# Kernel tuning notes

Measured on AMD Instinct MI355X. Metric: run time of the kernel, lower is better.

## Reference

```python
import jax, jax.numpy as jnp
import numpy as np

N = 10000      # nodes
E = 320000     # edges (avg degree 32)
D = 512        # input features
H = 2048       # dim_hidden hard-coded in module
C = 40         # num_classes


def setup_inputs() -> dict:
    key = jax.random.key(0)
    k = jax.random.split(key, 4)
    x = jax.random.normal(k[0], (N, D), dtype=jnp.float32)
    edge_index = jax.random.randint(k[1], (2, E), 0, N)
    W1 = jax.random.normal(k[2], (D, H), dtype=jnp.float32) * (1.0 / np.sqrt(D))
    b1 = jnp.zeros((H,), jnp.float32)
    W2 = jax.random.normal(k[3], (H, C), dtype=jnp.float32) * (1.0 / np.sqrt(H))
    b2 = jnp.zeros((C,), jnp.float32)
    return {"x": x, "edge_index": edge_index, "W1": W1, "b1": b1, "W2": W2, "b2": b2}


def _sym_norm(edge_index, n):
    # GCN symmetric normalization with self-loops: deg includes the self loop.
    src, dst = edge_index[0], edge_index[1]
    deg = jnp.zeros((n,), jnp.float32).at[dst].add(1.0) + 1.0
    dinv = jax.lax.rsqrt(deg)
    return src, dst, dinv


def _propagate(h, src, dst, dinv):
    # out[i] = sum_{j->i} dinv[j]*dinv[i]*h[j]  +  dinv[i]^2 * h[i] (self loop)
    coef = (dinv[src] * dinv[dst])[:, None]            # [E,1]
    agg = jax.ops.segment_sum(h[src] * coef, dst, num_segments=h.shape[0])
    return agg + h * (dinv * dinv)[:, None]


def _gcn_conv(x, W, b, src, dst, dinv):
    # A_hat (X W) == (A_hat X) W; aggregate in the smaller feature dim.
    if W.shape[0] <= W.shape[1]:
        return _propagate(x, src, dst, dinv) @ W + b
    return _propagate(x @ W, src, dst, dinv) + b


def reference(x, edge_index, W1, b1, W2, b2):
    src, dst, dinv = _sym_norm(edge_index, x.shape[0])
    h = jax.nn.relu(_gcn_conv(x, W1, b1, src, dst, dinv))
    return _gcn_conv(h, W2, b2, src, dst, dinv)
```

## Files before the change

kernel.cpp:

```cpp
#include <hip/hip_runtime.h>
#include <stdint.h>

#define N_NODES 10000
#define N_EDGES 320000
#define D_IN    512
#define D_HID   2048
#define N_CLS   40
#define MP1     10112
#define HSTR    136

typedef float f32x4  __attribute__((ext_vector_type(4)));
typedef short bf16x8 __attribute__((ext_vector_type(8)));
typedef unsigned short us8 __attribute__((ext_vector_type(8)));

__device__ inline unsigned short f2bf(float f){
  unsigned int u = __float_as_uint(f);
  u += 0x7fffu + ((u >> 16) & 1u);
  return (unsigned short)(u >> 16);
}

__device__ inline float bf2f(unsigned short h){
  return __uint_as_float(((unsigned int)h) << 16);
}

__device__ inline void gl_lds16(const void* g, void* l){
  __builtin_amdgcn_global_load_lds((const __attribute__((address_space(1))) void*)g,
                                   (__attribute__((address_space(3))) void*)l, 16, 0, 0);
}

__global__ void k_prep0(const float* __restrict__ x, unsigned short* __restrict__ Xb,
                        const int* __restrict__ ei, int* __restrict__ deg){
  if (blockIdx.x < 2500){
    int idx = blockIdx.x*256 + threadIdx.x;
    const f32x4* x4 = (const f32x4*)x;
    f32x4 a = x4[idx*2], b = x4[idx*2+1];
    us8 o;
    o[0]=f2bf(a.x); o[1]=f2bf(a.y); o[2]=f2bf(a.z); o[3]=f2bf(a.w);
    o[4]=f2bf(b.x); o[5]=f2bf(b.y); o[6]=f2bf(b.z); o[7]=f2bf(b.w);
    *(us8*)(Xb + (size_t)idx*8) = o;
  } else {
    int e = (blockIdx.x - 2500)*256 + threadIdx.x;
    if (e < N_EDGES) atomicAdd(&deg[ei[N_EDGES + e]], 1);
  }
}

__global__ void k_scan(const int* __restrict__ deg, int* __restrict__ offsets,
                       int* __restrict__ cursor, float* __restrict__ dinv){
  __shared__ int sums[1024];
  const int t = threadIdx.x;
  const int CH = 10;
  int base = t*CH;
  int local[CH]; int s = 0;
  for (int j = 0; j < CH; j++){
    int v = (base + j < N_NODES) ? deg[base + j] : 0;
    local[j] = s; s += v;
    if (base + j < N_NODES) dinv[base + j] = rsqrtf((float)v + 1.0f);
  }
  sums[t] = s;
  __syncthreads();
  for (int off = 1; off < 1024; off <<= 1){
    int v = (t >= off) ? sums[t - off] : 0;
    __syncthreads();
    sums[t] += v;
    __syncthreads();
  }
  int pre = (t > 0) ? sums[t-1] : 0;
  for (int j = 0; j < CH; j++){
    int idx = base + j;
    if (idx < N_NODES){ int o = pre + local[j]; offsets[idx] = o; cursor[idx] = o; }
  }
}

__global__ void k_fill(const int* __restrict__ ei, int* __restrict__ cursor, int* __restrict__ csr_src){
  int e = blockIdx.x*256 + threadIdx.x;
  if (e < N_EDGES){
    int s = ei[e], d = ei[N_EDGES + e];
    int pos = atomicAdd(&cursor[d], 1);
    csr_src[pos] = s;
  }
}

__global__ __launch_bounds__(256) void k_gjoint(const unsigned short* __restrict__ Xb,
                          const int* __restrict__ csr_src,
                          const int* __restrict__ offsets, const int* __restrict__ deg,
                          const float* __restrict__ dinv, unsigned short* __restrict__ Pb,
                          const float* __restrict__ W1, unsigned short* __restrict__ Wt1,
                          const float* __restrict__ W2, unsigned short* __restrict__ Wt2){
  __shared__ float tile[32][33];
  if (blockIdx.x < 2500){
    const int w    = threadIdx.x >> 6;
    const int lane = threadIdx.x & 63;
    const int i    = blockIdx.x*4 + w;
    const float di = dinv[i];
    float acc[8];
    us8 xi = *(const us8*)(Xb + (size_t)i*D_IN + lane*8);
    const float dii = di*di;
    #pragma unroll
    for (int r = 0; r < 8; r++) acc[r] = dii * bf2f(xi[r]);
    const int start = offsets[i], cnt = deg[i];
    const unsigned short* Xl = Xb + lane*8;
    for (int c0 = 0; c0 < cnt; c0 += 64){
      int m = cnt - c0; if (m > 64) m = 64;
      int s = 0; float cf = 0.0f;
      if (lane < m){ s = csr_src[start + c0 + lane]; cf = dinv[s]*di; }
      int j = 0;
      for (; j + 8 <= m; j += 8){
        int   s0 = __shfl(s, j),   s1 = __shfl(s, j+1), s2 = __shfl(s, j+2), s3 = __shfl(s, j+3);
        int   s4 = __shfl(s, j+4), s5 = __shfl(s, j+5), s6 = __shfl(s, j+6), s7 = __shfl(s, j+7);
        float c0f = __shfl(cf, j),   c1f = __shfl(cf, j+1), c2f = __shfl(cf, j+2), c3f = __shfl(cf, j+3);
        float c4f = __shfl(cf, j+4), c5f = __shfl(cf, j+5), c6f = __shfl(cf, j+6), c7f = __shfl(cf, j+7);
        us8 x0 = *(const us8*)(Xl + (size_t)s0*D_IN);
        us8 x1 = *(const us8*)(Xl + (size_t)s1*D_IN);
        us8 x2 = *(const us8*)(Xl + (size_t)s2*D_IN);
        us8 x3 = *(const us8*)(Xl + (size_t)s3*D_IN);
        us8 x4 = *(const us8*)(Xl + (size_t)s4*D_IN);
        us8 x5 = *(const us8*)(Xl + (size_t)s5*D_IN);
        us8 x6 = *(const us8*)(Xl + (size_t)s6*D_IN);
        us8 x7 = *(const us8*)(Xl + (size_t)s7*D_IN);
        #pragma unroll
        for (int r = 0; r < 8; r++) acc[r] += c0f * bf2f(x0[r]);
        #pragma unroll
        for (int r = 0; r < 8; r++) acc[r] += c1f * bf2f(x1[r]);
        #pragma unroll
        for (int r = 0; r < 8; r++) acc[r] += c2f * bf2f(x2[r]);
        #pragma unroll
        for (int r = 0; r < 8; r++) acc[r] += c3f * bf2f(x3[r]);
        #pragma unroll
        for (int r = 0; r < 8; r++) acc[r] += c4f * bf2f(x4[r]);
        #pragma unroll
        for (int r = 0; r < 8; r++) acc[r] += c5f * bf2f(x5[r]);
        #pragma unroll
        for (int r = 0; r < 8; r++) acc[r] += c6f * bf2f(x6[r]);
        #pragma unroll
        for (int r = 0; r < 8; r++) acc[r] += c7f * bf2f(x7[r]);
      }
      for (; j < m; j++){
        int   sj = __shfl(s, j);
        float cj = __shfl(cf, j);
        us8 xr = *(const us8*)(Xl + (size_t)sj*D_IN);
        #pragma unroll
        for (int r = 0; r < 8; r++) acc[r] += cj * bf2f(xr[r]);
      }
    }
    us8 o;
    #pragma unroll
    for (int r = 0; r < 8; r++) o[r] = f2bf(acc[r]);
    *(us8*)(Pb + (size_t)i*D_IN + lane*8) = o;
  } else if (blockIdx.x < 2500 + 1024){
    const int bb = blockIdx.x - 2500;
    const int n0 = (bb & 63)*32, k0 = (bb >> 6)*32;
    const int tx = threadIdx.x & 31, ty = threadIdx.x >> 5;
    for (int i = 0; i < 32; i += 8)
      tile[ty+i][tx] = W1[(size_t)(k0+ty+i)*D_HID + n0+tx];
    __syncthreads();
    for (int i = 0; i < 32; i += 8)
      Wt1[(size_t)(n0+ty+i)*D_IN + k0+tx] = f2bf(tile[tx][ty+i]);
  } else {
    int idx = (blockIdx.x - 3524)*256 + threadIdx.x;
    if (idx < 48*D_HID){
      int n = idx >> 11, k = idx & (D_HID-1);
      Wt2[idx] = (n < N_CLS) ? f2bf(W2[k*N_CLS + n]) : (unsigned short)0;
    }
  }
}

__global__ __launch_bounds__(256, 4) void k_gemm1f(const unsigned short* __restrict__ Pb,
                                                   const unsigned short* __restrict__ Wt1,
                                                   const float* __restrict__ b1,
                                                   const unsigned short* __restrict__ Wt2,
                                                   float* __restrict__ Gp){
  __shared__ short smem[128*HSTR];
  short* Hs = smem;
  const int t    = threadIdx.x;
  const int lane = t & 63;
  const int wid  = t >> 6;
  const int wm   = (wid >> 1)*64, wn = (wid & 1)*64;
  const int m0   = blockIdx.y*128, n0 = blockIdx.x*128;
  const int arow = t >> 2;
  const int akof = ((t & 3) ^ ((t >> 3) & 3))*8;
  const int fr   = lane & 15;
  const int q    = lane >> 4;
  const int sq8  = (q ^ ((fr >> 1) & 3))*8;

  const unsigned short* ApA = Pb  + (size_t)(m0 +      arow)*D_IN + akof;
  const unsigned short* ApB = Pb  + (size_t)(m0 + 64 + arow)*D_IN + akof;
  const unsigned short* BpA = Wt1 + (size_t)(n0 +      arow)*D_IN + akof;
  const unsigned short* BpB = Wt1 + (size_t)(n0 + 64 + arow)*D_IN + akof;

  f32x4 acc[4][4] = {};
  {
    short* As = smem;       short* Bs = smem + 4096;
    gl_lds16(ApA, As + t*8);  gl_lds16(ApB, As + 2048 + t*8);
    gl_lds16(BpA, Bs + t*8);  gl_lds16(BpB, Bs + 2048 + t*8);
  }
  #pragma unroll
  for (int ks = 0; ks < 16; ks++){
    if (ks < 15){
      short* As = smem + ((ks+1)&1)*8192;
      short* Bs = As + 4096;
      const int kb = (ks+1)*32;
      gl_lds16(ApA + kb, As + t*8);  gl_lds16(ApB + kb, As + 2048 + t*8);
      gl_lds16(BpA + kb, Bs + t*8);  gl_lds16(BpB + kb, Bs + 2048 + t*8);
      asm volatile("" ::: "memory");
      __builtin_amdgcn_s_waitcnt(0x0F74);
    } else {
      asm volatile("" ::: "memory");
      __builtin_amdgcn_s_waitcnt(0x0F70);
    }
    __builtin_amdgcn_s_barrier();
    asm volatile("" ::: "memory");
    const short* As = smem + (ks&1)*8192;
    const short* Bs = As + 4096;
    bf16x8 a[4], b[4];
    #pragma unroll
    for (int i = 0; i < 4; i++) a[i] = *(const bf16x8*)(As + (wm + i*16 + fr)*32 + sq8);
    #pragma unroll
    for (int j = 0; j < 4; j++) b[j] = *(const bf16x8*)(Bs + (wn + j*16 + fr)*32 + sq8);
    #pragma unroll
    for (int i = 0; i < 4; i++)
      #pragma unroll
      for (int j = 0; j < 4; j++)
        acc[i][j] = __builtin_amdgcn_mfma_f32_16x16x32_bf16(a[i], b[j], acc[i][j], 0, 0, 0);
    asm volatile("" ::: "memory");
    __builtin_amdgcn_s_barrier();
    asm volatile("" ::: "memory");
  }
  #pragma unroll
  for (int j = 0; j < 4; j++){
    int col = wn + j*16 + fr;
    float bias = b1[n0 + col];
    #pragma unroll
    for (int i = 0; i < 4; i++){
      int rbase = wm + i*16 + q*4;
      f32x4 v = acc[i][j];
      #pragma unroll
      for (int r = 0; r < 4; r++){
        float h = fmaxf(v[r] + bias, 0.0f);
        Hs[(rbase + r)*HSTR + col] = (short)f2bf(h);
      }
    }
  }
  __syncthreads();
  f32x4 acc2[2][3] = {};
  for (int ks = 0; ks < 4; ks++){
    bf16x8 a2[2];
    #pragma unroll
    for (int i2 = 0; i2 < 2; i2++)
      a2[i2] = *(const bf16x8*)(Hs + (wid*32 + i2*16 + fr)*HSTR + ks*32 + q*8);
    #pragma unroll
    for (int j2 = 0; j2 < 3; j2++){
      bf16x8 b2 = *(const bf16x8*)(Wt2 + (size_t)(j2*16 + fr)*D_HID + n0 + ks*32 + q*8);
      #pragma unroll
      for (int i2 = 0; i2 < 2; i2++)
        acc2[i2][j2] = __builtin_amdgcn_mfma_f32_16x16x32_bf16(a2[i2], b2, acc2[i2][j2], 0, 0, 0);
    }
  }
  float* Gpp = Gp + (size_t)blockIdx.x*N_NODES*N_CLS;
  #pragma unroll
  for (int j2 = 0; j2 < 3; j2++){
    int col = j2*16 + fr;
    if (col < N_CLS){
      #pragma unroll
      for (int i2 = 0; i2 < 2; i2++){
        int rbase = m0 + wid*32 + i2*16 + q*4;
        f32x4 v = acc2[i2][j2];
        #pragma unroll
        for (int r = 0; r < 4; r++){
          int row = rbase + r;
          if (row < N_NODES)
            Gpp[(size_t)row*N_CLS + col] = v[r];
        }
      }
    }
  }
}

__global__ void k_reduceG(const float* __restrict__ Gp, float* __restrict__ G){
  int idx = blockIdx.x*256 + threadIdx.x;
  if (idx < N_NODES*N_CLS){
    float s = 0.0f;
    #pragma unroll
    for (int p = 0; p < 16; p++)
      s += Gp[(size_t)p*N_NODES*N_CLS + idx];
    G[idx] = s;
  }
}

__global__ void k_gather2(const float* __restrict__ G, const int* __restrict__ csr_src,
                          const int* __restrict__ offsets, const int* __restrict__ deg,
                          const float* __restrict__ dinv, const float* __restrict__ b2,
                          float* __restrict__ out){
  __shared__ int   ssrc[64];
  __shared__ float scoef[64];
  const int i = blockIdx.x;
  const int t = threadIdx.x;
  const float di = dinv[i];
  const int start = offsets[i], cnt = deg[i];
  float acc = 0.0f;
  if (t < N_CLS) acc = di*di * G[i*N_CLS + t];
  for (int c0 = 0; c0 < cnt; c0 += 64){
    int m = cnt - c0; if (m > 64) m = 64;
    if (t < m){
      int s = csr_src[start + c0 + t];
      ssrc[t] = s; scoef[t] = dinv[s]*di;
    }
    __syncthreads();
    if (t < N_CLS)
      for (int j = 0; j < m; j++)
        acc += scoef[j] * G[ssrc[j]*N_CLS + t];
    __syncthreads();
  }
  if (t < N_CLS) out[i*N_CLS + t] = acc + b2[t];
}

extern "C" void kernel_launch(void* const* d_in, const int* in_sizes, int n_in,
                              void* d_out, int out_size, void* d_ws, size_t ws_size,
                              hipStream_t stream){
  const float* x  = (const float*)d_in[0];
  const int*   ei = (const int*)d_in[1];
  const float* W1 = (const float*)d_in[2];
  const float* b1 = (const float*)d_in[3];
  const float* W2 = (const float*)d_in[4];
  const float* b2 = (const float*)d_in[5];
  float* out = (float*)d_out;

  char* ws = (char*)d_ws;
  size_t off = 0;
  auto alloc = [&](size_t bytes) -> void* {
    void* p = ws + off; off += (bytes + 255) & ~(size_t)255; return p;
  };
  int*   deg     = (int*)alloc((size_t)N_NODES*4);
  float* dinv    = (float*)alloc((size_t)N_NODES*4);
  int*   offsets = (int*)alloc((size_t)N_NODES*4);
  int*   cursor  = (int*)alloc((size_t)N_NODES*4);
  int*   csr     = (int*)alloc((size_t)N_EDGES*4);
  unsigned short* Xb  = (unsigned short*)alloc((size_t)N_NODES*D_IN*2);
  unsigned short* Pb  = (unsigned short*)alloc((size_t)MP1*D_IN*2);
  unsigned short* Wt1 = (unsigned short*)alloc((size_t)D_HID*D_IN*2);
  unsigned short* Wt2 = (unsigned short*)alloc((size_t)48*D_HID*2);
  float* G  = (float*)alloc((size_t)N_NODES*N_CLS*4);
  float* Gp = (float*)alloc((size_t)16*N_NODES*N_CLS*4);

  hipMemsetAsync(deg, 0, (size_t)N_NODES*4, stream);

  k_prep0<<<2500 + 1250, 256, 0, stream>>>(x, Xb, ei, deg);
  k_scan<<<1, 1024, 0, stream>>>(deg, offsets, cursor, dinv);
  k_fill<<<(N_EDGES+255)/256, 256, 0, stream>>>(ei, cursor, csr);
  k_gjoint<<<2500 + 1024 + 384, 256, 0, stream>>>(Xb, csr, offsets, deg, dinv, Pb,
                                                  W1, Wt1, W2, Wt2);
  k_gemm1f<<<dim3(D_HID/128, MP1/128), 256, 0, stream>>>(Pb, Wt1, b1, Wt2, Gp);
  k_reduceG<<<(N_NODES*N_CLS + 255)/256, 256, 0, stream>>>(Gp, G);
  k_gather2<<<N_NODES, 64, 0, stream>>>(G, csr, offsets, deg, dinv, b2, out);
}
```

Before: 217.4 us.

## Enlarge GEMM1 tile to 256x128 with 512 threads and drop offsets array

The first GEMM block tile grows from 128x128 with 4 waves to 256x128 with 8 waves. Each block now loads one shared 128-row B tile plus two A halves per k-step, so every Wt1 tile is reused across more rows and the number of global-to-LDS loads per output element falls. The padded row count grows from 10112 to 10240 to fit the larger tile, and the epilogue's shared-memory H staging buffer doubles in size. Separately, the scan kernel no longer writes an offsets array: the gather kernels rebuild each node's start as the post-fill cursor minus its degree, which saves one store and one buffer.

Result: no change. 215.3 us (-0.9%).

```diff
diff --git a/kernel.cpp b/kernel.cpp
--- a/kernel.cpp
+++ b/kernel.cpp
@@ -6,7 +6,7 @@
 #define D_IN    512
 #define D_HID   2048
 #define N_CLS   40
-#define MP1     10112
+#define MP2     10240
 #define HSTR    136
 
 typedef float f32x4  __attribute__((ext_vector_type(4)));
@@ -44,17 +44,23 @@
   }
 }
 
-__global__ void k_scan(const int* __restrict__ deg, int* __restrict__ offsets,
-                       int* __restrict__ cursor, float* __restrict__ dinv){
+__global__ void k_scan(const int* __restrict__ deg, int* __restrict__ cursor,
+                       float* __restrict__ dinv){
+  __shared__ int sdeg[N_NODES];
   __shared__ int sums[1024];
   const int t = threadIdx.x;
+  for (int j = t; j < N_NODES; j += 1024){
+    int v = deg[j];
+    sdeg[j] = v;
+    dinv[j] = rsqrtf((float)v + 1.0f);
+  }
+  __syncthreads();
   const int CH = 10;
   int base = t*CH;
   int local[CH]; int s = 0;
   for (int j = 0; j < CH; j++){
-    int v = (base + j < N_NODES) ? deg[base + j] : 0;
+    int v = (base + j < N_NODES) ? sdeg[base + j] : 0;
     local[j] = s; s += v;
-    if (base + j < N_NODES) dinv[base + j] = rsqrtf((float)v + 1.0f);
   }
   sums[t] = s;
   __syncthreads();
@@ -67,8 +73,10 @@
   int pre = (t > 0) ? sums[t-1] : 0;
   for (int j = 0; j < CH; j++){
     int idx = base + j;
-    if (idx < N_NODES){ int o = pre + local[j]; offsets[idx] = o; cursor[idx] = o; }
-  }
+    if (idx < N_NODES) sdeg[idx] = pre + local[j];
+  }
+  __syncthreads();
+  for (int j = t; j < N_NODES; j += 1024) cursor[j] = sdeg[j];
 }
 
 __global__ void k_fill(const int* __restrict__ ei, int* __restrict__ cursor, int* __restrict__ csr_src){
@@ -82,7 +90,7 @@
 
 __global__ __launch_bounds__(256) void k_gjoint(const unsigned short* __restrict__ Xb,
                           const int* __restrict__ csr_src,
-                          const int* __restrict__ offsets, const int* __restrict__ deg,
+                          const int* __restrict__ cursor, const int* __restrict__ deg,
                           const float* __restrict__ dinv, unsigned short* __restrict__ Pb,
                           const float* __restrict__ W1, unsigned short* __restrict__ Wt1,
                           const float* __restrict__ W2, unsigned short* __restrict__ Wt2){
@@ -97,7 +105,8 @@
     const float dii = di*di;
     #pragma unroll
     for (int r = 0; r < 8; r++) acc[r] = dii * bf2f(xi[r]);
-    const int start = offsets[i], cnt = deg[i];
+    const int cnt = deg[i];
+    const int start = cursor[i] - cnt;
     const unsigned short* Xl = Xb + lane*8;
     for (int c0 = 0; c0 < cnt; c0 += 64){
       int m = cnt - c0; if (m > 64) m = 64;
@@ -164,53 +173,53 @@
   }
 }
 
-__global__ __launch_bounds__(256, 4) void k_gemm1f(const unsigned short* __restrict__ Pb,
+__global__ __launch_bounds__(512, 4) void k_gemm1f(const unsigned short* __restrict__ Pb,
                                                    const unsigned short* __restrict__ Wt1,
                                                    const float* __restrict__ b1,
                                                    const unsigned short* __restrict__ Wt2,
                                                    float* __restrict__ Gp){
-  __shared__ short smem[128*HSTR];
+  __shared__ short smem[256*HSTR];
   short* Hs = smem;
   const int t    = threadIdx.x;
   const int lane = t & 63;
   const int wid  = t >> 6;
-  const int wm   = (wid >> 1)*64, wn = (wid & 1)*64;
-  const int m0   = blockIdx.y*128, n0 = blockIdx.x*128;
+  const int wm   = (wid >> 1)*64;
+  const int wn   = (wid & 1)*64;
+  const int m0   = blockIdx.y*256, n0 = blockIdx.x*128;
   const int arow = t >> 2;
   const int akof = ((t & 3) ^ ((t >> 3) & 3))*8;
   const int fr   = lane & 15;
   const int q    = lane >> 4;
   const int sq8  = (q ^ ((fr >> 1) & 3))*8;
 
-  const unsigned short* ApA = Pb  + (size_t)(m0 +      arow)*D_IN + akof;
-  const unsigned short* ApB = Pb  + (size_t)(m0 + 64 + arow)*D_IN + akof;
-  const unsigned short* BpA = Wt1 + (size_t)(n0 +      arow)*D_IN + akof;
-  const unsigned short* BpB = Wt1 + (size_t)(n0 + 64 + arow)*D_IN + akof;
+  const unsigned short* ApA = Pb  + (size_t)(m0 +       arow)*D_IN + akof;
+  const unsigned short* ApB = Pb  + (size_t)(m0 + 128 + arow)*D_IN + akof;
+  const unsigned short* BpA = Wt1 + (size_t)(n0 +       arow)*D_IN + akof;
 
   f32x4 acc[4][4] = {};
   {
-    short* As = smem;       short* Bs = smem + 4096;
-    gl_lds16(ApA, As + t*8);  gl_lds16(ApB, As + 2048 + t*8);
-    gl_lds16(BpA, Bs + t*8);  gl_lds16(BpB, Bs + 2048 + t*8);
+    gl_lds16(ApA, smem + t*8);
+    gl_lds16(ApB, smem + 4096 + t*8);
+    gl_lds16(BpA, smem + 8192 + t*8);
   }
   #pragma unroll
   for (int ks = 0; ks < 16; ks++){
     if (ks < 15){
-      short* As = smem + ((ks+1)&1)*8192;
-      short* Bs = As + 4096;
+      short* buf = smem + ((ks+1)&1)*12288;
       const int kb = (ks+1)*32;
-      gl_lds16(ApA + kb, As + t*8);  gl_lds16(ApB + kb, As + 2048 + t*8);
-      gl_lds16(BpA + kb, Bs + t*8);  gl_lds16(BpB + kb, Bs + 2048 + t*8);
+      gl_lds16(ApA + kb, buf + t*8);
+      gl_lds16(ApB + kb, buf + 4096 + t*8);
+      gl_lds16(BpA + kb, buf + 8192 + t*8);
       asm volatile("" ::: "memory");
-      __builtin_amdgcn_s_waitcnt(0x0F74);
+      __builtin_amdgcn_s_waitcnt(0x0F73);
     } else {
       asm volatile("" ::: "memory");
       __builtin_amdgcn_s_waitcnt(0x0F70);
     }
     __builtin_amdgcn_s_barrier();
     asm volatile("" ::: "memory");
-    const short* As = smem + (ks&1)*8192;
-    const short* Bs = As + 4096;
+    const short* As = smem + (ks&1)*12288;
+    const short* Bs = As + 8192;
     bf16x8 a[4], b[4];
     #pragma unroll
     for (int i = 0; i < 4; i++) a[i] = *(const bf16x8*)(As + (wm + i*16 + fr)*32 + sq8);
@@ -287,7 +296,7 @@
 }
 
 __global__ void k_gather2(const float* __restrict__ G, const int* __restrict__ csr_src,
-                          const int* __restrict__ offsets, const int* __restrict__ deg,
+                          const int* __restrict__ cursor, const int* __restrict__ deg,
                           const float* __restrict__ dinv, const float* __restrict__ b2,
                           float* __restrict__ out){
   __shared__ int   ssrc[64];
@@ -295,7 +304,8 @@
   const int i = blockIdx.x;
   const int t = threadIdx.x;
   const float di = dinv[i];
-  const int start = offsets[i], cnt = deg[i];
+  const int cnt = deg[i];
+  const int start = cursor[i] - cnt;
   float acc = 0.0f;
   if (t < N_CLS) acc = di*di * G[i*N_CLS + t];
   for (int c0 = 0; c0 < cnt; c0 += 64){
@@ -331,11 +341,10 @@
   };
   int*   deg     = (int*)alloc((size_t)N_NODES*4);
   float* dinv    = (float*)alloc((size_t)N_NODES*4);
-  int*   offsets = (int*)alloc((size_t)N_NODES*4);
   int*   cursor  = (int*)alloc((size_t)N_NODES*4);
   int*   csr     = (int*)alloc((size_t)N_EDGES*4);
   unsigned short* Xb  = (unsigned short*)alloc((size_t)N_NODES*D_IN*2);
-  unsigned short* Pb  = (unsigned short*)alloc((size_t)MP1*D_IN*2);
+  unsigned short* Pb  = (unsigned short*)alloc((size_t)MP2*D_IN*2);
   unsigned short* Wt1 = (unsigned short*)alloc((size_t)D_HID*D_IN*2);
   unsigned short* Wt2 = (unsigned short*)alloc((size_t)48*D_HID*2);
   float* G  = (float*)alloc((size_t)N_NODES*N_CLS*4);
@@ -344,11 +353,11 @@
   hipMemsetAsync(deg, 0, (size_t)N_NODES*4, stream);
 
   k_prep0<<<2500 + 1250, 256, 0, stream>>>(x, Xb, ei, deg);
-  k_scan<<<1, 1024, 0, stream>>>(deg, offsets, cursor, dinv);
+  k_scan<<<1, 1024, 0, stream>>>(deg, cursor, dinv);
   k_fill<<<(N_EDGES+255)/256, 256, 0, stream>>>(ei, cursor, csr);
-  k_gjoint<<<2500 + 1024 + 384, 256, 0, stream>>>(Xb, csr, offsets, deg, dinv, Pb,
+  k_gjoint<<<2500 + 1024 + 384, 256, 0, stream>>>(Xb, csr, cursor, deg, dinv, Pb,
                                                   W1, Wt1, W2, Wt2);
-  k_gemm1f<<<dim3(D_HID/128, MP1/128), 256, 0, stream>>>(Pb, Wt1, b1, Wt2, Gp);
+  k_gemm1f<<<dim3(D_HID/128, MP2/256), 512, 0, stream>>>(Pb, Wt1, b1, Wt2, Gp);
   k_reduceG<<<(N_NODES*N_CLS + 255)/256, 256, 0, stream>>>(Gp, G);
-  k_gather2<<<N_NODES, 64, 0, stream>>>(G, csr, offsets, deg, dinv, b2, out);
-}
+  k_gather2<<<N_NODES, 64, 0, stream>>>(G, csr, cursor, deg, dinv, b2, out);
+}
```
